# Performance work log

Measured on AMD Instinct MI355X. Metric: run time of the kernel, lower is better.

The kernel has to match this reference:

```python
import jax, jax.numpy as jnp
import numpy as np

N_NODES = 50000
N_EDGES = 1600000
IN_CH = 128
HID = 128  # 2 * out_channels
NUM_GRAPHS = 64


def gcn_conv(x, row, col, ew, W, b, num_nodes):
    # PyG GCNConv: add self-loops (weight 1), symmetric degree norm, x @ W,
    # gather at source row, scale by norm, scatter-add at target col, add bias.
    loop = jnp.arange(num_nodes)
    r = jnp.concatenate([row, loop])
    c = jnp.concatenate([col, loop])
    w = jnp.concatenate([ew, jnp.ones((num_nodes,), ew.dtype)])
    deg = jax.ops.segment_sum(w, c, num_segments=num_nodes)
    dis = jnp.where(deg > 0, jax.lax.rsqrt(jnp.where(deg > 0, deg, 1.0)), 0.0)
    norm = dis[r] * w * dis[c]  # [E+N]
    xw = x @ W  # [N, HID]
    msg = xw[r] * norm[:, None]  # [E+N, HID] gather + scale
    out = jax.ops.segment_sum(msg, c, num_segments=num_nodes)
    return out + b


def setup_inputs() -> dict:
    key = jax.random.key(0)
    ks = jax.random.split(key, 8)
    x = jax.random.normal(ks[0], (N_NODES, IN_CH), dtype=jnp.float32)
    edge_index = jax.random.randint(ks[1], (2, N_EDGES), 0, N_NODES, dtype=jnp.int64)
    edge_weight = jax.random.uniform(ks[2], (N_EDGES,), dtype=jnp.float32)
    batch = jnp.sort(jax.random.randint(ks[3], (N_NODES,), 0, NUM_GRAPHS, dtype=jnp.int64))
    W1 = jax.random.normal(ks[4], (IN_CH, HID), dtype=jnp.float32) * 0.01
    b1 = jnp.zeros((HID,), jnp.float32)
    W2 = jax.random.normal(ks[5], (HID, HID), dtype=jnp.float32) * 0.01
    b2 = jnp.zeros((HID,), jnp.float32)
    return {"x": x, "edge_index": edge_index, "edge_weight": edge_weight,
            "batch": batch, "W1": W1, "b1": b1, "W2": W2, "b2": b2}


def reference(x, edge_index, edge_weight, batch, W1, b1, W2, b2):
    row, col = edge_index[0], edge_index[1]
    h = jax.nn.relu(gcn_conv(x, row, col, edge_weight, W1, b1, N_NODES))
    h = jax.nn.relu(gcn_conv(h, row, col, edge_weight, W2, b2, N_NODES))
    # global_mean_pool over batch segment ids
    sums = jax.ops.segment_sum(h, batch, num_segments=NUM_GRAPHS)
    cnts = jax.ops.segment_sum(jnp.ones((N_NODES,), h.dtype), batch, num_segments=NUM_GRAPHS)
    pooled = sums / jnp.maximum(cnts, 1.0)[:, None]
    return h, pooled
```

## Files before the change

kernel.cpp:

```cpp
#include <hip/hip_runtime.h>


#define CH 128
#define BSH 7
#define NBLK 1024
#define MAXNB 512
#define PCH 32

static __device__ __forceinline__ unsigned short f2bf(float f) {
    unsigned u = __float_as_uint(f);
    unsigned r = (u + 0x7FFF + ((u >> 16) & 1)) >> 16;
    return (unsigned short)r;
}

__global__ __launch_bounds__(256) void k_sort1a(const int* __restrict__ col,
                                                int* __restrict__ H, int E, int NB, int chunk) {
    __shared__ int hist[MAXNB];
    int t = threadIdx.x, blk = blockIdx.x;
    for (int i = t; i < NB; i += 256) hist[i] = 0;
    __syncthreads();
    int s = blk * chunk, e1 = min(s + chunk, E);
    for (int e = s + t; e < e1; e += 256) atomicAdd(&hist[col[e] >> BSH], 1);
    __syncthreads();
    for (int i = t; i < NB; i += 256) H[(size_t)i * NBLK + blk] = hist[i];
}

__global__ __launch_bounds__(1024) void k_scan1(int* __restrict__ data,
                                                int* __restrict__ bsum, int n) {
    __shared__ int sd[1024];
    int t = threadIdx.x;
    int i = blockIdx.x * 1024 + t;
    int v = (i < n) ? data[i] : 0;
    sd[t] = v;
    __syncthreads();
    for (int off = 1; off < 1024; off <<= 1) {
        int u = (t >= off) ? sd[t - off] : 0;
        __syncthreads();
        sd[t] += u;
        __syncthreads();
    }
    if (i < n) data[i] = sd[t] - v;
    if (t == 1023) bsum[blockIdx.x] = sd[1023];
}

__global__ __launch_bounds__(1024) void k_scan2(int* bsum, int nb, int* total) {
    __shared__ int sd[1024];
    int t = threadIdx.x;
    int v = (t < nb) ? bsum[t] : 0;
    sd[t] = v;
    __syncthreads();
    for (int off = 1; off < 1024; off <<= 1) {
        int u = (t >= off) ? sd[t - off] : 0;
        __syncthreads();
        sd[t] += u;
        __syncthreads();
    }
    if (t < nb) bsum[t] = sd[t] - v;
    if (t == 1023) *total = sd[1023];
}

__global__ void k_scan3(int* data, const int* __restrict__ bsum, int n) {
    int i = blockIdx.x * 256 + threadIdx.x;
    if (i < n) data[i] += bsum[i >> 10];
}

__global__ __launch_bounds__(256) void k_sort1b(const int* __restrict__ row,
                                                const int* __restrict__ col,
                                                const float* __restrict__ ew,
                                                const int* __restrict__ Hs,
                                                int2* __restrict__ pairs2,
                                                int E, int NB, int chunk) {
    __shared__ int cur[MAXNB];
    int t = threadIdx.x, blk = blockIdx.x;
    for (int i = t; i < NB; i += 256) cur[i] = Hs[(size_t)i * NBLK + blk];
    __syncthreads();
    int s = blk * chunk, e1 = min(s + chunk, E);
    for (int e = s + t; e < e1; e += 256) {
        int c = col[e];
        int pos = atomicAdd(&cur[c >> BSH], 1);
        pairs2[pos] = make_int2(row[e] | ((c & 127) << 17), __float_as_int(ew[e]));
    }
}

__global__ __launch_bounds__(256) void k_sort2(const int* __restrict__ Hs,
                                               const int2* __restrict__ pairs2,
                                               int2* __restrict__ pairs,
                                               int* __restrict__ rowptr,
                                               float* __restrict__ dis,
                                               int E, int N, int NB) {
    __shared__ int hist[128];
    __shared__ int pref[128];
    __shared__ float wsum[128];
    int b = blockIdx.x, t = threadIdx.x;
    int n0 = b << BSH;
    int s = Hs[(size_t)b * NBLK];
    int e1 = (b + 1 < NB) ? Hs[(size_t)(b + 1) * NBLK] : E;
    if (t < 128) { hist[t] = 0; wsum[t] = 0.f; }
    __syncthreads();
    for (int e = s + t; e < e1; e += 256)
        atomicAdd(&hist[(unsigned)pairs2[e].x >> 17], 1);
    __syncthreads();
    if (t < 128) pref[t] = hist[t];
    __syncthreads();
    for (int off = 1; off < 128; off <<= 1) {
        int v = 0;
        if (t < 128 && t >= off) v = pref[t - off];
        __syncthreads();
        if (t < 128) pref[t] += v;
        __syncthreads();
    }
    if (t < 128) {
        int excl = pref[t] - hist[t];
        int node = n0 + t;
        if (node < N) rowptr[node] = s + excl;
        hist[t] = s + excl;
    }
    if (b == NB - 1 && t == 0) rowptr[N] = E;
    __syncthreads();
    for (int e = s + t; e < e1; e += 256) {
        int2 pr = pairs2[e];
        int li = (unsigned)pr.x >> 17;
        int pos = atomicAdd(&hist[li], 1);
        pairs[pos] = make_int2(pr.x & 0x1FFFF, pr.y);
        atomicAdd(&wsum[li], __int_as_float(pr.y));
    }
    __syncthreads();
    if (t < 128 && n0 + t < N) dis[n0 + t] = rsqrtf(1.0f + wsum[t]);
}

__global__ __launch_bounds__(64) void k_norm(const int* __restrict__ rowptr,
                                             int2* __restrict__ pairs,
                                             const float* __restrict__ dis, int N) {
    int n = blockIdx.x;
    int lane = threadIdx.x;
    float dn = dis[n];
    int e0 = rowptr[n], e1 = rowptr[n + 1];
    for (int e = e0 + lane; e < e1; e += 64) {
        int2 p = pairs[e];
        float nn = dn * __int_as_float(p.y) * dis[p.x];
        pairs[e].y = __float_as_int(nn);
    }
}

__global__ __launch_bounds__(256) void k_gemm(const float* __restrict__ X,
                                              const float* __restrict__ W,
                                              unsigned short* __restrict__ Y, int N) {
    __shared__ float Ws[128][128];
    __shared__ float Xs[32][128];
    int tid = threadIdx.x;
    {
        const float4* Wv = (const float4*)W;
        float4* Sv = (float4*)&Ws[0][0];
#pragma unroll
        for (int i = 0; i < 16; ++i) Sv[tid + 256 * i] = Wv[tid + 256 * i];
    }
    int row0 = blockIdx.x * 32;
    {
        float4* Xsv = (float4*)&Xs[0][0];
        if (row0 + 32 <= N) {
            const float4* Xv = (const float4*)(X + (size_t)row0 * CH);
#pragma unroll
            for (int i = 0; i < 4; ++i) { int idx = tid + 256 * i; Xsv[idx] = Xv[idx]; }
        } else {
#pragma unroll
            for (int i = 0; i < 4; ++i) {
                int idx = tid + 256 * i;
                int r = idx >> 5;
                float4 v = make_float4(0.f, 0.f, 0.f, 0.f);
                if (row0 + r < N) v = ((const float4*)(X + (size_t)(row0 + r) * CH))[idx & 31];
                Xsv[idx] = v;
            }
        }
    }
    __syncthreads();
    int c4 = tid & 31;
    int rl = tid >> 5;
    float4 acc[4];
#pragma unroll
    for (int j = 0; j < 4; ++j) acc[j] = make_float4(0.f, 0.f, 0.f, 0.f);
    for (int k = 0; k < 128; k += 4) {
        float4 w0 = *(const float4*)&Ws[k + 0][c4 * 4];
        float4 w1 = *(const float4*)&Ws[k + 1][c4 * 4];
        float4 w2 = *(const float4*)&Ws[k + 2][c4 * 4];
        float4 w3 = *(const float4*)&Ws[k + 3][c4 * 4];
#pragma unroll
        for (int j = 0; j < 4; ++j) {
            float4 xv = *(const float4*)&Xs[rl + 8 * j][k];
            acc[j].x += xv.x * w0.x + xv.y * w1.x + xv.z * w2.x + xv.w * w3.x;
            acc[j].y += xv.x * w0.y + xv.y * w1.y + xv.z * w2.y + xv.w * w3.y;
            acc[j].z += xv.x * w0.z + xv.y * w1.z + xv.z * w2.z + xv.w * w3.z;
            acc[j].w += xv.x * w0.w + xv.y * w1.w + xv.z * w2.w + xv.w * w3.w;
        }
    }
#pragma unroll
    for (int j = 0; j < 4; ++j) {
        int r = row0 + rl + 8 * j;
        if (r < N) {
            ushort4 o;
            o.x = f2bf(acc[j].x); o.y = f2bf(acc[j].y);
            o.z = f2bf(acc[j].z); o.w = f2bf(acc[j].w);
            *(ushort4*)&Y[(size_t)r * CH + c4 * 4] = o;
        }
    }
}

__global__ __launch_bounds__(64) void k_agg(const unsigned int* __restrict__ XW,
                                            const float* __restrict__ dis,
                                            const int* __restrict__ rowptr,
                                            const int2* __restrict__ pairs,
                                            const float* __restrict__ bias,
                                            float* __restrict__ OUT, int N) {
    int n = blockIdx.x;
    if (n >= N) return;
    int lane = threadIdx.x;
    float d = dis[n];
    float sn = d * d;
    unsigned a = XW[(size_t)n * 64 + lane];
    float ax = __uint_as_float(a << 16) * sn;
    float ay = __uint_as_float(a & 0xFFFF0000u) * sn;
    int e0 = rowptr[n], e1 = rowptr[n + 1];
    int e = e0;
    for (; e + 4 <= e1; e += 4) {
        int2 p0 = pairs[e], p1 = pairs[e + 1], p2 = pairs[e + 2], p3 = pairs[e + 3];
        unsigned v0 = XW[(size_t)p0.x * 64 + lane];
        unsigned v1 = XW[(size_t)p1.x * 64 + lane];
        unsigned v2 = XW[(size_t)p2.x * 64 + lane];
        unsigned v3 = XW[(size_t)p3.x * 64 + lane];
        float n0 = __int_as_float(p0.y), n1 = __int_as_float(p1.y);
        float n2 = __int_as_float(p2.y), n3 = __int_as_float(p3.y);
        ax += n0 * __uint_as_float(v0 << 16) + n1 * __uint_as_float(v1 << 16)
            + n2 * __uint_as_float(v2 << 16) + n3 * __uint_as_float(v3 << 16);
        ay += n0 * __uint_as_float(v0 & 0xFFFF0000u) + n1 * __uint_as_float(v1 & 0xFFFF0000u)
            + n2 * __uint_as_float(v2 & 0xFFFF0000u) + n3 * __uint_as_float(v3 & 0xFFFF0000u);
    }
    for (; e < e1; ++e) {
        int2 p = pairs[e];
        unsigned v = XW[(size_t)p.x * 64 + lane];
        float nn = __int_as_float(p.y);
        ax += nn * __uint_as_float(v << 16);
        ay += nn * __uint_as_float(v & 0xFFFF0000u);
    }
    float2 b = ((const float2*)bias)[lane];
    ax = fmaxf(ax + b.x, 0.f);
    ay = fmaxf(ay + b.y, 0.f);
    ((float2*)OUT)[(size_t)n * 64 + lane] = make_float2(ax, ay);
}

__device__ __forceinline__ int lowerb(const int* a, int n, int v) {
    int lo = 0, hi = n;
    while (lo < hi) {
        int m = (lo + hi) >> 1;
        if (a[m] < v) lo = m + 1; else hi = m;
    }
    return lo;
}

__global__ __launch_bounds__(128) void k_pool1(const float* __restrict__ H,
                                               const int* __restrict__ batch,
                                               float* __restrict__ partial, int N) {
    __shared__ int ss[2];
    int g = blockIdx.x / PCH;
    int k = blockIdx.x % PCH;
    if (threadIdx.x == 0) {
        ss[0] = lowerb(batch, N, g);
        ss[1] = lowerb(batch, N, g + 1);
    }
    __syncthreads();
    int s = ss[0], len = ss[1] - ss[0];
    int cs = s + (int)(((long long)len * k) / PCH);
    int ce = s + (int)(((long long)len * (k + 1)) / PCH);
    int ch = threadIdx.x;
    float a0 = 0.f, a1 = 0.f;
    int n = cs;
    for (; n + 2 <= ce; n += 2) {
        a0 += H[(size_t)(n + 0) * CH + ch];
        a1 += H[(size_t)(n + 1) * CH + ch];
    }
    for (; n < ce; ++n) a0 += H[(size_t)n * CH + ch];
    partial[(size_t)blockIdx.x * CH + ch] = a0 + a1;
}

__global__ __launch_bounds__(128) void k_pool2(const float* __restrict__ partial,
                                               const int* __restrict__ batch,
                                               float* __restrict__ P, int N) {
    __shared__ int ss[2];
    int g = blockIdx.x;
    if (threadIdx.x == 0) {
        ss[0] = lowerb(batch, N, g);
        ss[1] = lowerb(batch, N, g + 1);
    }
    __syncthreads();
    int ch = threadIdx.x;
    float a = 0.f;
#pragma unroll
    for (int k = 0; k < PCH; ++k) a += partial[(size_t)(g * PCH + k) * CH + ch];
    float c = (float)(ss[1] - ss[0]);
    P[(size_t)g * CH + ch] = a / fmaxf(c, 1.f);
}

extern "C" void kernel_launch(void* const* d_in, const int* in_sizes, int n_in,
                              void* d_out, int out_size, void* d_ws, size_t ws_size,
                              hipStream_t stream) {
    const float* x     = (const float*)d_in[0];
    const int*   ei    = (const int*)d_in[1];
    const float* ew    = (const float*)d_in[2];
    const int*   batch = (const int*)d_in[3];
    const float* W1    = (const float*)d_in[4];
    const float* b1    = (const float*)d_in[5];
    const float* W2    = (const float*)d_in[6];
    const float* b2    = (const float*)d_in[7];

    int N = in_sizes[0] / CH;
    int E = in_sizes[1] / 2;
    const int* row = ei;
    const int* col = ei + E;

    float* out    = (float*)d_out;
    float* h      = out;
    float* pooled = out + (size_t)N * CH;

    int NB    = (N + 127) >> BSH;
    int chunk = (E + NBLK - 1) / NBLK;
    int n2    = NB * NBLK;

    char* wsb = (char*)d_ws;
    size_t oN  = ((size_t)N * 4 + 255) & ~(size_t)255;
    size_t oN1 = ((size_t)(N + 1) * 4 + 255) & ~(size_t)255;
    size_t oH  = ((size_t)(n2 + 1) * 4 + 255) & ~(size_t)255;
    size_t oB  = 4096;
    size_t oE2 = ((size_t)E * 8 + 255) & ~(size_t)255;
    float* dis    = (float*)wsb;
    int*   rowptr = (int*)(wsb + oN);
    int*   H      = (int*)(wsb + oN + oN1);
    int*   bsum   = (int*)(wsb + oN + oN1 + oH);
    int2*  pairs  = (int2*)(wsb + oN + oN1 + oH + oB);
    unsigned short* xw = (unsigned short*)(wsb + oN + oN1 + oH + oB + oE2);
    int2*  pairs2 = (int2*)xw;
    float* partial = (float*)H;

    int sb2 = (n2 + 1023) / 1024;

    k_sort1a<<<NBLK, 256, 0, stream>>>(col, H, E, NB, chunk);
    k_scan1<<<sb2, 1024, 0, stream>>>(H, bsum, n2);
    k_scan2<<<1, 1024, 0, stream>>>(bsum, sb2, H + n2);
    k_scan3<<<(n2 + 255) / 256, 256, 0, stream>>>(H, bsum, n2);
    k_sort1b<<<NBLK, 256, 0, stream>>>(row, col, ew, H, pairs2, E, NB, chunk);
    k_sort2<<<NB, 256, 0, stream>>>(H, pairs2, pairs, rowptr, dis, E, N, NB);
    k_norm<<<N, 64, 0, stream>>>(rowptr, pairs, dis, N);

    int gb = (N + 31) / 32;
    k_gemm<<<gb, 256, 0, stream>>>(x, W1, xw, N);
    k_agg<<<N, 64, 0, stream>>>((const unsigned int*)xw, dis, rowptr, pairs, b1, h, N);
    k_gemm<<<gb, 256, 0, stream>>>(h, W2, xw, N);
    k_agg<<<N, 64, 0, stream>>>((const unsigned int*)xw, dis, rowptr, pairs, b2, h, N);
    k_pool1<<<64 * PCH, 128, 0, stream>>>(h, batch, partial, N);
    k_pool2<<<64, 128, 0, stream>>>(partial, batch, pooled, N);
}
```

Measured before the change: 261.3 us.

## Use bf16 MFMA GEMM, fold scan fixup and edge norm into consumers

Replaces the FP32 SIMT GEMM with a bf16 MFMA 16x16x32 kernel that keeps a transposed, padded bf16 copy of W in LDS and converts X to bf16 on load. It also drops the scan-fixup kernel by adding the block sums inside the sort kernels, and drops the separate edge-normalization pass by computing dis[src]*w*dis[dst] inline during aggregation. The aggregation loop is unrolled to 8 edges. This saves kernel launches and one full read-write pass over the edge list. In exchange each aggregation now does an extra dis gather per edge, and X is rounded to bf16 before the matmul, which lowers precision.

```diff
diff --git a/kernel.cpp b/kernel.cpp
--- a/kernel.cpp
+++ b/kernel.cpp
@@ -6,12 +6,18 @@
 #define NBLK 1024
 #define MAXNB 512
 #define PCH 32
+#define LDW 136
+
+typedef __attribute__((ext_vector_type(8))) short bf16x8;
+typedef __attribute__((ext_vector_type(4))) float f32x4;
 
 static __device__ __forceinline__ unsigned short f2bf(float f) {
     unsigned u = __float_as_uint(f);
     unsigned r = (u + 0x7FFF + ((u >> 16) & 1)) >> 16;
     return (unsigned short)r;
 }
+static __device__ __forceinline__ float bflo(unsigned v) { return __uint_as_float(v << 16); }
+static __device__ __forceinline__ float bfhi(unsigned v) { return __uint_as_float(v & 0xFFFF0000u); }
 
 __global__ __launch_bounds__(256) void k_sort1a(const int* __restrict__ col,
                                                 int* __restrict__ H, int E, int NB, int chunk) {
@@ -59,20 +65,16 @@
     if (t == 1023) *total = sd[1023];
 }
 
-__global__ void k_scan3(int* data, const int* __restrict__ bsum, int n) {
-    int i = blockIdx.x * 256 + threadIdx.x;
-    if (i < n) data[i] += bsum[i >> 10];
-}
-
 __global__ __launch_bounds__(256) void k_sort1b(const int* __restrict__ row,
                                                 const int* __restrict__ col,
                                                 const float* __restrict__ ew,
                                                 const int* __restrict__ Hs,
+                                                const int* __restrict__ bsum,
                                                 int2* __restrict__ pairs2,
                                                 int E, int NB, int chunk) {
     __shared__ int cur[MAXNB];
     int t = threadIdx.x, blk = blockIdx.x;
-    for (int i = t; i < NB; i += 256) cur[i] = Hs[(size_t)i * NBLK + blk];
+    for (int i = t; i < NB; i += 256) cur[i] = Hs[(size_t)i * NBLK + blk] + bsum[i];
     __syncthreads();
     int s = blk * chunk, e1 = min(s + chunk, E);
     for (int e = s + t; e < e1; e += 256) {
@@ -83,6 +85,7 @@
 }
 
 __global__ __launch_bounds__(256) void k_sort2(const int* __restrict__ Hs,
+                                               const int* __restrict__ bsum,
                                                const int2* __restrict__ pairs2,
                                                int2* __restrict__ pairs,
                                                int* __restrict__ rowptr,
@@ -93,8 +96,8 @@
     __shared__ float wsum[128];
     int b = blockIdx.x, t = threadIdx.x;
     int n0 = b << BSH;
-    int s = Hs[(size_t)b * NBLK];
-    int e1 = (b + 1 < NB) ? Hs[(size_t)(b + 1) * NBLK] : E;
+    int s = Hs[(size_t)b * NBLK] + bsum[b];
+    int e1 = (b + 1 < NB) ? Hs[(size_t)(b + 1) * NBLK] + bsum[b + 1] : E;
     if (t < 128) { hist[t] = 0; wsum[t] = 0.f; }
     __syncthreads();
     for (int e = s + t; e < e1; e += 256)
@@ -128,78 +131,53 @@
     if (t < 128 && n0 + t < N) dis[n0 + t] = rsqrtf(1.0f + wsum[t]);
 }
 
-__global__ __launch_bounds__(64) void k_norm(const int* __restrict__ rowptr,
-                                             int2* __restrict__ pairs,
-                                             const float* __restrict__ dis, int N) {
-    int n = blockIdx.x;
-    int lane = threadIdx.x;
-    float dn = dis[n];
-    int e0 = rowptr[n], e1 = rowptr[n + 1];
-    for (int e = e0 + lane; e < e1; e += 64) {
-        int2 p = pairs[e];
-        float nn = dn * __int_as_float(p.y) * dis[p.x];
-        pairs[e].y = __float_as_int(nn);
-    }
-}
-
-__global__ __launch_bounds__(256) void k_gemm(const float* __restrict__ X,
+__global__ __launch_bounds__(512) void k_gemm(const float* __restrict__ X,
                                               const float* __restrict__ W,
                                               unsigned short* __restrict__ Y, int N) {
-    __shared__ float Ws[128][128];
-    __shared__ float Xs[32][128];
+    __shared__ unsigned short Wt[128 * LDW];
     int tid = threadIdx.x;
-    {
-        const float4* Wv = (const float4*)W;
-        float4* Sv = (float4*)&Ws[0][0];
-#pragma unroll
-        for (int i = 0; i < 16; ++i) Sv[tid + 256 * i] = Wv[tid + 256 * i];
-    }
-    int row0 = blockIdx.x * 32;
-    {
-        float4* Xsv = (float4*)&Xs[0][0];
-        if (row0 + 32 <= N) {
-            const float4* Xv = (const float4*)(X + (size_t)row0 * CH);
-#pragma unroll
-            for (int i = 0; i < 4; ++i) { int idx = tid + 256 * i; Xsv[idx] = Xv[idx]; }
+    for (int i = tid; i < 4096; i += 512) {
+        float4 v = ((const float4*)W)[i];
+        int k = i >> 5;
+        int c = (i & 31) * 4;
+        Wt[(c + 0) * LDW + k] = f2bf(v.x);
+        Wt[(c + 1) * LDW + k] = f2bf(v.y);
+        Wt[(c + 2) * LDW + k] = f2bf(v.z);
+        Wt[(c + 3) * LDW + k] = f2bf(v.w);
+    }
+    __syncthreads();
+    int w = tid >> 6, lane = tid & 63;
+    int l15 = lane & 15, kg = lane >> 4;
+    int r = blockIdx.x * 128 + w * 16 + l15;
+    f32x4 acc[8];
+#pragma unroll
+    for (int ct = 0; ct < 8; ++ct) acc[ct] = (f32x4){0.f, 0.f, 0.f, 0.f};
+#pragma unroll
+    for (int kb = 0; kb < 128; kb += 32) {
+        union { unsigned u[4]; bf16x8 v; } a;
+        if (r < N) {
+            const float4* xp = (const float4*)(X + (size_t)r * CH + kb + kg * 8);
+            float4 x0 = xp[0], x1 = xp[1];
+            a.u[0] = ((unsigned)f2bf(x0.y) << 16) | f2bf(x0.x);
+            a.u[1] = ((unsigned)f2bf(x0.w) << 16) | f2bf(x0.z);
+            a.u[2] = ((unsigned)f2bf(x1.y) << 16) | f2bf(x1.x);
+            a.u[3] = ((unsigned)f2bf(x1.w) << 16) | f2bf(x1.z);
         } else {
-#pragma unroll
-            for (int i = 0; i < 4; ++i) {
-                int idx = tid + 256 * i;
-                int r = idx >> 5;
-                float4 v = make_float4(0.f, 0.f, 0.f, 0.f);
-                if (row0 + r < N) v = ((const float4*)(X + (size_t)(row0 + r) * CH))[idx & 31];
-                Xsv[idx] = v;
-            }
+            a.u[0] = a.u[1] = a.u[2] = a.u[3] = 0;
         }
-    }
-    __syncthreads();
-    int c4 = tid & 31;
-    int rl = tid >> 5;
-    float4 acc[4];
-#pragma unroll
-    for (int j = 0; j < 4; ++j) acc[j] = make_float4(0.f, 0.f, 0.f, 0.f);
-    for (int k = 0; k < 128; k += 4) {
-        float4 w0 = *(const float4*)&Ws[k + 0][c4 * 4];
-        float4 w1 = *(const float4*)&Ws[k + 1][c4 * 4];
-        float4 w2 = *(const float4*)&Ws[k + 2][c4 * 4];
-        float4 w3 = *(const float4*)&Ws[k + 3][c4 * 4];
+#pragma unroll
+        for (int ct = 0; ct < 8; ++ct) {
+            bf16x8 b = *(const bf16x8*)&Wt[(ct * 16 + l15) * LDW + kb + kg * 8];
+            acc[ct] = __builtin_amdgcn_mfma_f32_16x16x32_bf16(a.v, b, acc[ct], 0, 0, 0);
+        }
+    }
+    int orow = blockIdx.x * 128 + w * 16 + kg * 4;
+#pragma unroll
+    for (int ct = 0; ct < 8; ++ct) {
 #pragma unroll
         for (int j = 0; j < 4; ++j) {
-            float4 xv = *(const float4*)&Xs[rl + 8 * j][k];
-            acc[j].x += xv.x * w0.x + xv.y * w1.x + xv.z * w2.x + xv.w * w3.x;
-            acc[j].y += xv.x * w0.y + xv.y * w1.y + xv.z * w2.y + xv.w * w3.y;
-            acc[j].z += xv.x * w0.z + xv.y * w1.z + xv.z * w2.z + xv.w * w3.z;
-            acc[j].w += xv.x * w0.w + xv.y * w1.w + xv.z * w2.w + xv.w * w3.w;
-        }
-    }
-#pragma unroll
-    for (int j = 0; j < 4; ++j) {
-        int r = row0 + rl + 8 * j;
-        if (r < N) {
-            ushort4 o;
-            o.x = f2bf(acc[j].x); o.y = f2bf(acc[j].y);
-            o.z = f2bf(acc[j].z); o.w = f2bf(acc[j].w);
-            *(ushort4*)&Y[(size_t)r * CH + c4 * 4] = o;
+            int rr = orow + j;
+            if (rr < N) Y[(size_t)rr * CH + ct * 16 + l15] = f2bf(acc[ct][j]);
         }
     }
 }
@@ -213,32 +191,43 @@
     int n = blockIdx.x;
     if (n >= N) return;
     int lane = threadIdx.x;
-    float d = dis[n];
-    float sn = d * d;
+    float dn = dis[n];
+    float sn = dn * dn;
     unsigned a = XW[(size_t)n * 64 + lane];
-    float ax = __uint_as_float(a << 16) * sn;
-    float ay = __uint_as_float(a & 0xFFFF0000u) * sn;
+    float ax = bflo(a) * sn;
+    float ay = bfhi(a) * sn;
     int e0 = rowptr[n], e1 = rowptr[n + 1];
     int e = e0;
-    for (; e + 4 <= e1; e += 4) {
-        int2 p0 = pairs[e], p1 = pairs[e + 1], p2 = pairs[e + 2], p3 = pairs[e + 3];
+    for (; e + 8 <= e1; e += 8) {
+        int2 p0 = pairs[e],     p1 = pairs[e + 1], p2 = pairs[e + 2], p3 = pairs[e + 3];
+        int2 p4 = pairs[e + 4], p5 = pairs[e + 5], p6 = pairs[e + 6], p7 = pairs[e + 7];
         unsigned v0 = XW[(size_t)p0.x * 64 + lane];
         unsigned v1 = XW[(size_t)p1.x * 64 + lane];
         unsigned v2 = XW[(size_t)p2.x * 64 + lane];
         unsigned v3 = XW[(size_t)p3.x * 64 + lane];
-        float n0 = __int_as_float(p0.y), n1 = __int_as_float(p1.y);
-        float n2 = __int_as_float(p2.y), n3 = __int_as_float(p3.y);
-        ax += n0 * __uint_as_float(v0 << 16) + n1 * __uint_as_float(v1 << 16)
-            + n2 * __uint_as_float(v2 << 16) + n3 * __uint_as_float(v3 << 16);
-        ay += n0 * __uint_as_float(v0 & 0xFFFF0000u) + n1 * __uint_as_float(v1 & 0xFFFF0000u)
-            + n2 * __uint_as_float(v2 & 0xFFFF0000u) + n3 * __uint_as_float(v3 & 0xFFFF0000u);
+        unsigned v4 = XW[(size_t)p4.x * 64 + lane];
+        unsigned v5 = XW[(size_t)p5.x * 64 + lane];
+        unsigned v6 = XW[(size_t)p6.x * 64 + lane];
+        unsigned v7 = XW[(size_t)p7.x * 64 + lane];
+        float n0 = dn * __int_as_float(p0.y) * dis[p0.x];
+        float n1 = dn * __int_as_float(p1.y) * dis[p1.x];
+        float n2 = dn * __int_as_float(p2.y) * dis[p2.x];
+        float n3 = dn * __int_as_float(p3.y) * dis[p3.x];
+        float n4 = dn * __int_as_float(p4.y) * dis[p4.x];
+        float n5 = dn * __int_as_float(p5.y) * dis[p5.x];
+        float n6 = dn * __int_as_float(p6.y) * dis[p6.x];
+        float n7 = dn * __int_as_float(p7.y) * dis[p7.x];
+        ax += n0 * bflo(v0) + n1 * bflo(v1) + n2 * bflo(v2) + n3 * bflo(v3)
+            + n4 * bflo(v4) + n5 * bflo(v5) + n6 * bflo(v6) + n7 * bflo(v7);
+        ay += n0 * bfhi(v0) + n1 * bfhi(v1) + n2 * bfhi(v2) + n3 * bfhi(v3)
+            + n4 * bfhi(v4) + n5 * bfhi(v5) + n6 * bfhi(v6) + n7 * bfhi(v7);
     }
     for (; e < e1; ++e) {
         int2 p = pairs[e];
         unsigned v = XW[(size_t)p.x * 64 + lane];
-        float nn = __int_as_float(p.y);
-        ax += nn * __uint_as_float(v << 16);
-        ay += nn * __uint_as_float(v & 0xFFFF0000u);
+        float nn = dn * __int_as_float(p.y) * dis[p.x];
+        ax += nn * bflo(v);
+        ay += nn * bfhi(v);
     }
     float2 b = ((const float2*)bias)[lane];
     ax = fmaxf(ax + b.x, 0.f);
@@ -343,15 +332,13 @@
     k_sort1a<<<NBLK, 256, 0, stream>>>(col, H, E, NB, chunk);
     k_scan1<<<sb2, 1024, 0, stream>>>(H, bsum, n2);
     k_scan2<<<1, 1024, 0, stream>>>(bsum, sb2, H + n2);
-    k_scan3<<<(n2 + 255) / 256, 256, 0, stream>>>(H, bsum, n2);
-    k_sort1b<<<NBLK, 256, 0, stream>>>(row, col, ew, H, pairs2, E, NB, chunk);
-    k_sort2<<<NB, 256, 0, stream>>>(H, pairs2, pairs, rowptr, dis, E, N, NB);
-    k_norm<<<N, 64, 0, stream>>>(rowptr, pairs, dis, N);
-
-    int gb = (N + 31) / 32;
-    k_gemm<<<gb, 256, 0, stream>>>(x, W1, xw, N);
+    k_sort1b<<<NBLK, 256, 0, stream>>>(row, col, ew, H, bsum, pairs2, E, NB, chunk);
+    k_sort2<<<NB, 256, 0, stream>>>(H, bsum, pairs2, pairs, rowptr, dis, E, N, NB);
+
+    int gb = (N + 127) / 128;
+    k_gemm<<<gb, 512, 0, stream>>>(x, W1, xw, N);
     k_agg<<<N, 64, 0, stream>>>((const unsigned int*)xw, dis, rowptr, pairs, b1, h, N);
-    k_gemm<<<gb, 256, 0, stream>>>(h, W2, xw, N);
+    k_gemm<<<gb, 512, 0, stream>>>(h, W2, xw, N);
     k_agg<<<N, 64, 0, stream>>>((const unsigned int*)xw, dis, rowptr, pairs, b2, h, N);
     k_pool1<<<64 * PCH, 128, 0, stream>>>(h, batch, partial, N);
     k_pool2<<<64, 128, 0, stream>>>(partial, batch, pooled, N);
```

Result: faster. 225.0 us (-13.9%).
